# Optimization experiments

Hardware: AMD Instinct MI355X
Metric: run time of the kernel (lower is better)

## Reference

```python
import jax, jax.numpy as jnp
import numpy as np
from jax import lax

T = 32768
DUNITS = 1024
ATT_DIM = 512
EPROJS = 512
ACONV_CHANS = 32
ACONV_FILTS = 15  # kernel = 2*15+1 = 31


def setup_inputs() -> dict:
    key = jax.random.key(0)
    ks = jax.random.split(key, 8)
    dec_z = jax.random.normal(ks[0], (1, DUNITS), jnp.float32)
    att_prev = jax.random.uniform(ks[1], (1, T), jnp.float32)
    att_prev = att_prev / jnp.sum(att_prev, axis=1, keepdims=True)  # prob-like alignment
    pre_compute_enc_h = jax.random.normal(ks[2], (1, T, ATT_DIM), jnp.float32) * 0.1
    enc_h = jax.random.normal(ks[3], (1, T, EPROJS), jnp.float32)
    mask = jnp.zeros((1, T), jnp.float32)  # additive mask (0 = keep)
    conv_w = jax.random.normal(ks[4], (ACONV_CHANS, 1, 2 * ACONV_FILTS + 1), jnp.float32) * 0.1
    conv_b = jnp.zeros((ACONV_CHANS,), jnp.float32)
    W_att = jax.random.normal(ks[5], (ATT_DIM, ACONV_CHANS), jnp.float32) * 0.1
    W_dec = jax.random.normal(ks[6], (ATT_DIM, DUNITS), jnp.float32) * 0.03
    W_g = jax.random.normal(ks[7], (1, ATT_DIM), jnp.float32) * 0.05
    b_g = jnp.zeros((1,), jnp.float32)
    return {"dec_z": dec_z, "att_prev": att_prev, "pre_compute_enc_h": pre_compute_enc_h,
            "enc_h": enc_h, "mask": mask, "conv_w": conv_w, "conv_b": conv_b,
            "W_att": W_att, "W_dec": W_dec, "W_g": W_g, "b_g": b_g}


def reference(dec_z, att_prev, pre_compute_enc_h, enc_h, mask, conv_w, conv_b, W_att, W_dec, W_g, b_g):
    scaling = 2.0
    # location conv: att_prev [1,T] -> [1,C,T] (Conv2d with height-1 kernel == Conv1d)
    att_conv = lax.conv_general_dilated(
        att_prev[:, None, :], conv_w, window_strides=(1,),
        padding=[(ACONV_FILTS, ACONV_FILTS)],
        dimension_numbers=("NCH", "OIH", "NCH"))
    att_conv = att_conv + conv_b[None, :, None]          # [1,C,T]
    att_conv = jnp.einsum("bct,ac->bta", att_conv, W_att)  # mlp_att -> [1,T,att_dim]
    dec_z_tiled = (dec_z @ W_dec.T)[:, None, :]           # [1,1,att_dim]
    # gvec over tanh sum -> energies [1,T]
    e = jnp.einsum("bta,a->bt", jnp.tanh(pre_compute_enc_h + dec_z_tiled + att_conv), W_g[0]) + b_g[0]
    e = e + mask
    w = jax.nn.softmax(scaling * e, axis=1)               # [1,T]
    # forward-attention recurrence: shift-add-mul, then L1 normalize
    att_prev_shift = jnp.pad(att_prev, ((0, 0), (1, 0)))[:, :-1]
    w = (att_prev + att_prev_shift) * w
    w = jnp.clip(w, 1e-6, None)
    w = w / jnp.sum(w, axis=1, keepdims=True)             # L1 normalize (w > 0)
    c = jnp.sum(enc_h * w[:, :, None], axis=1)            # [1,eprojs]
    return (c, w)
```

## Files before the change

kernel.cpp:

```cpp
#include <hip/hip_runtime.h>

#define T_LEN 32768
#define ADIM  512
#define NDEC  1024
#define KTAPS 31

#define WS_BASE 0
#define WS_G    512
#define WS_SARR 16384
#define WS_BMAX 49152
#define WS_BSUM 51200
#define WS_SSUM 53248
#define WS_U    53504
#define WS_CREP 86272

typedef __attribute__((ext_vector_type(8))) short bf16x8;
typedef __attribute__((ext_vector_type(4))) float f32x4;

__device__ __forceinline__ float fast_tanh(float x) {
    float e = __expf(2.0f * x);
    return 1.0f - 2.0f * __builtin_amdgcn_rcpf(e + 1.0f);
}

__device__ __forceinline__ unsigned short f2bf(float f) {
    unsigned u = __float_as_uint(f);
    return (unsigned short)((u + 0x7FFFu + ((u >> 16) & 1u)) >> 16);
}

__global__ __launch_bounds__(256) void k0_prep(
        const float* __restrict__ dec_z, const float* __restrict__ conv_w,
        const float* __restrict__ conv_b, const float* __restrict__ W_att,
        const float* __restrict__ W_dec, float* __restrict__ ws) {
    int b = blockIdx.x, tid = threadIdx.x;
    int lane = tid & 63, wave = tid >> 6;
    if (b < 64) {
        if (b == 0 && tid == 0) ws[WS_SSUM] = 0.f;
        for (int s = 0; s < 2; ++s) {
            int a = b * 8 + wave * 2 + s;
            float sum = 0.f;
            #pragma unroll
            for (int i = 0; i < 16; ++i)
                sum += W_dec[a * NDEC + i * 64 + lane] * dec_z[i * 64 + lane];
            #pragma unroll
            for (int off = 32; off > 0; off >>= 1) sum += __shfl_xor(sum, off);
            if (lane == 0) {
                float bias = 0.f;
                #pragma unroll
                for (int c = 0; c < 32; ++c) bias += conv_b[c] * W_att[a * 32 + c];
                ws[WS_BASE + a] = sum + bias;
            }
        }
    } else {
        int k = b - 64;
        unsigned short* Gf = (unsigned short*)(ws + WS_G);
        for (int s = 0; s < 2; ++s) {
            int a = 2 * tid + s;
            float g = 0.f;
            if (k < KTAPS) {
                #pragma unroll
                for (int c = 0; c < 32; ++c)
                    g += conv_w[c * KTAPS + k] * W_att[a * 32 + c];
            }
            int at = a >> 4, col = a & 15;
            int l = col | ((k >> 3) << 4), i = k & 7;
            Gf[(at * 64 + l) * 8 + i] = f2bf(g);
        }
    }
}

__global__ __launch_bounds__(512, 8) void k1_energy(
        const float* __restrict__ att_prev, const float* __restrict__ pre,
        const float* __restrict__ mask, const float* __restrict__ W_g,
        const float* __restrict__ b_g, float* __restrict__ ws) {
    __shared__ float pre_s[16 * ADIM];
    __shared__ float ap_s[48];
    __shared__ float eP[8][16];
    int tid = threadIdx.x, lane = tid & 63, wave = tid >> 6;
    int t0 = blockIdx.x * 16;

    if (blockIdx.x < 32) ws[WS_CREP + blockIdx.x * 512 + tid] = 0.f;

    {
        const float* grow = pre + (size_t)(t0 + 2 * wave) * ADIM + lane * 4;
        float* lrow = &pre_s[(2 * wave) * ADIM];
        #pragma unroll
        for (int r = 0; r < 2; ++r) {
            #pragma unroll
            for (int h = 0; h < 2; ++h) {
                __builtin_amdgcn_global_load_lds(
                    (const __attribute__((address_space(1))) void*)(grow + r * ADIM + h * 256),
                    (__attribute__((address_space(3))) void*)(lrow + r * ADIM + h * 256),
                    16, 0, 0);
            }
        }
    }
    if (tid < 48) {
        int g = t0 - 15 + tid;
        ap_s[tid] = (g >= 0 && g < T_LEN) ? att_prev[g] : 0.f;
    }
    __syncthreads();

    int row = lane & 15, g4 = lane >> 4;

    bf16x8 afrag;
    int aidx = row + g4 * 8;
    #pragma unroll
    for (int i = 0; i < 8; ++i) afrag[i] = (short)f2bf(ap_s[aidx + i]);

    const unsigned short* Gf = (const unsigned short*)(ws + WS_G);
    float e_acc[4] = {0.f, 0.f, 0.f, 0.f};

    #pragma unroll 2
    for (int p = 0; p < 4; ++p) {
        int at = wave * 4 + p;
        int ac = at * 16 + row;
        bf16x8 bfrag = *(const bf16x8*)(Gf + (size_t)(at * 64 + lane) * 8);
        float bs = ws[WS_BASE + ac];
        f32x4 c = {bs, bs, bs, bs};
        c = __builtin_amdgcn_mfma_f32_16x16x32_bf16(afrag, bfrag, c, 0, 0, 0);
        float wgv = W_g[ac];
        #pragma unroll
        for (int r = 0; r < 4; ++r) {
            float pv = pre_s[(g4 * 4 + r) * ADIM + ac];
            e_acc[r] = fmaf(fast_tanh(c[r] + pv), wgv, e_acc[r]);
        }
    }

    #pragma unroll
    for (int r = 0; r < 4; ++r) {
        float s = e_acc[r];
        s += __shfl_xor(s, 1); s += __shfl_xor(s, 2);
        s += __shfl_xor(s, 4); s += __shfl_xor(s, 8);
        e_acc[r] = s;
    }
    if (row == 0) {
        #pragma unroll
        for (int r = 0; r < 4; ++r) eP[wave][g4 * 4 + r] = e_acc[r];
    }
    __syncthreads();

    if (wave == 0) {
        float sv = -1e30f, z0 = 0.f;
        if (lane < 16) {
            float e = 0.f;
            #pragma unroll
            for (int q = 0; q < 8; ++q) e += eP[q][lane];
            int t = t0 + lane;
            sv = 2.0f * (e + b_g[0] + mask[t]);
            ws[WS_SARR + t] = sv;
            z0 = 1.0f;
        }
        float m = sv, z = z0;
        #pragma unroll
        for (int off = 32; off > 0; off >>= 1) {
            float mo = __shfl_xor(m, off), zo = __shfl_xor(z, off);
            float mn = fmaxf(m, mo);
            z = z * __expf(m - mn) + zo * __expf(mo - mn);
            m = mn;
        }
        if (lane == 0) { ws[WS_BMAX + blockIdx.x] = m; ws[WS_BSUM + blockIdx.x] = z; }
    }
}

__global__ __launch_bounds__(512, 4) void k3_context(
        const float* __restrict__ att_prev, const float* __restrict__ enc_h,
        float* __restrict__ ws) {
    __shared__ float wmz[16];
    __shared__ float cbuf[4 * 512];
    int tid = threadIdx.x, lane = tid & 63, wave = tid >> 6;

    float mo[4], zo[4];
    #pragma unroll
    for (int k = 0; k < 4; ++k) {
        mo[k] = ws[WS_BMAX + (wave + 8 * k) * 64 + lane];
        zo[k] = ws[WS_BSUM + (wave + 8 * k) * 64 + lane];
    }
    float m = mo[0], z = zo[0];
    #pragma unroll
    for (int k = 1; k < 4; ++k) {
        float mn = fmaxf(m, mo[k]);
        z = z * __expf(m - mn) + zo[k] * __expf(mo[k] - mn);
        m = mn;
    }
    #pragma unroll
    for (int off = 32; off > 0; off >>= 1) {
        float mx = __shfl_xor(m, off), zx = __shfl_xor(z, off);
        float mn = fmaxf(m, mx);
        z = z * __expf(m - mn) + zx * __expf(mx - mn);
        m = mn;
    }
    if (lane == 0) { wmz[wave] = m; wmz[8 + wave] = z; }
    __syncthreads();
    float M = wmz[0], Z = wmz[8];
    #pragma unroll
    for (int w = 1; w < 8; ++w) {
        float mn = fmaxf(M, wmz[w]);
        Z = Z * __expf(M - mn) + wmz[8 + w] * __expf(wmz[w] - mn);
        M = mn;
    }
    float invZ = 1.0f / Z;

    int team = tid >> 7, l = tid & 127;
    int a4 = 4 * l;
    float4 acc = make_float4(0.f, 0.f, 0.f, 0.f);

    #pragma unroll 1
    for (int half = 0; half < 2; ++half) {
        int t0 = blockIdx.x * 64 + half * 32;
        int tb = t0 + team * 8;

        float u[8];
        #pragma unroll
        for (int i = 0; i < 8; ++i) {
            int t = tb + i;
            float ap0 = att_prev[t];
            float apm = (t > 0) ? att_prev[t - 1] : 0.f;
            u[i] = fmaxf((ap0 + apm) * __expf(ws[WS_SARR + t] - M) * invZ, 1e-6f);
        }
        float4 e[8];
        #pragma unroll
        for (int i = 0; i < 8; ++i)
            e[i] = *(const float4*)(enc_h + (size_t)(tb + i) * ADIM + a4);
        #pragma unroll
        for (int i = 0; i < 8; ++i) {
            acc.x = fmaf(u[i], e[i].x, acc.x);
            acc.y = fmaf(u[i], e[i].y, acc.y);
            acc.z = fmaf(u[i], e[i].z, acc.z);
            acc.w = fmaf(u[i], e[i].w, acc.w);
        }

        if (wave == 0 && lane < 32) {
            int t = t0 + lane;
            float ap0 = att_prev[t];
            float apm = (t > 0) ? att_prev[t - 1] : 0.f;
            float uu = fmaxf((ap0 + apm) * __expf(ws[WS_SARR + t] - M) * invZ, 1e-6f);
            ws[WS_U + t] = uu;
            float s = uu;
            #pragma unroll
            for (int off = 16; off > 0; off >>= 1) s += __shfl_xor(s, off, 32);
            if (lane == 0) atomicAdd(&ws[WS_SSUM], s);
        }
    }

    if (team != 0) *(float4*)&cbuf[team * 512 + a4] = acc;
    __syncthreads();
    if (team == 0) {
        float4 b1 = *(const float4*)&cbuf[1 * 512 + a4];
        float4 b2 = *(const float4*)&cbuf[2 * 512 + a4];
        float4 b3 = *(const float4*)&cbuf[3 * 512 + a4];
        float* rep = ws + WS_CREP + (blockIdx.x & 31) * 512;
        atomicAdd(&rep[a4 + 0], acc.x + b1.x + b2.x + b3.x);
        atomicAdd(&rep[a4 + 1], acc.y + b1.y + b2.y + b3.y);
        atomicAdd(&rep[a4 + 2], acc.z + b1.z + b2.z + b3.z);
        atomicAdd(&rep[a4 + 3], acc.w + b1.w + b2.w + b3.w);
    }
}

__global__ __launch_bounds__(512) void k4_final(
        const float* __restrict__ ws, float* __restrict__ out) {
    int b = blockIdx.x, tid = threadIdx.x;
    float invS = 1.0f / ws[WS_SSUM];
    if (b == 0) {
        float acc = 0.f;
        #pragma unroll
        for (int r = 0; r < 32; ++r) acc += ws[WS_CREP + r * 512 + tid];
        out[tid] = acc * invS;
    } else {
        int i = (b - 1) * 512 + tid;
        out[512 + i] = ws[WS_U + i] * invS;
    }
}

extern "C" void kernel_launch(void* const* d_in, const int* in_sizes, int n_in,
                              void* d_out, int out_size, void* d_ws, size_t ws_size,
                              hipStream_t stream) {
    const float* dec_z    = (const float*)d_in[0];
    const float* att_prev = (const float*)d_in[1];
    const float* pre      = (const float*)d_in[2];
    const float* enc_h    = (const float*)d_in[3];
    const float* mask     = (const float*)d_in[4];
    const float* conv_w   = (const float*)d_in[5];
    const float* conv_b   = (const float*)d_in[6];
    const float* W_att    = (const float*)d_in[7];
    const float* W_dec    = (const float*)d_in[8];
    const float* W_g      = (const float*)d_in[9];
    const float* b_g      = (const float*)d_in[10];
    float* out = (float*)d_out;
    float* ws  = (float*)d_ws;

    k0_prep   <<<96,   256, 0, stream>>>(dec_z, conv_w, conv_b, W_att, W_dec, ws);
    k1_energy <<<2048, 512, 0, stream>>>(att_prev, pre, mask, W_g, b_g, ws);
    k3_context<<<512,  512, 0, stream>>>(att_prev, enc_h, ws);
    k4_final  <<<65,   512, 0, stream>>>(ws, out);
}
```

Baseline: 181.8 us.

## Give each wave its own 16 timesteps with double-buffered LDS prefetch

Restructures the energy kernel so each wave owns 16 timesteps and walks all 512 attention columns in four chunks. Chunks of pre_compute_enc_h stream into per-wave double-buffered LDS through async global-to-LDS loads with explicit vmcnt waits. This overlaps memory traffic with MFMA and tanh work and removes block-level syncs and the cross-wave energy reduction. The cost is fewer, larger blocks (512 blocks of 256 threads), lower occupancy, and hand-placed waitcnt/sched_barrier ordering that must exactly match the outstanding loads.

```diff
diff --git a/kernel.cpp b/kernel.cpp
--- a/kernel.cpp
+++ b/kernel.cpp
@@ -26,6 +26,13 @@
     unsigned u = __float_as_uint(f);
     return (unsigned short)((u + 0x7FFFu + ((u >> 16) & 1u)) >> 16);
 }
+
+#define WAITV8()  do { asm volatile("s_waitcnt vmcnt(8)" ::: "memory"); \
+                       __builtin_amdgcn_sched_barrier(0); } while (0)
+#define WAITV0()  do { asm volatile("s_waitcnt vmcnt(0)" ::: "memory"); \
+                       __builtin_amdgcn_sched_barrier(0); } while (0)
+#define WAITL0()  do { asm volatile("s_waitcnt lgkmcnt(0)" ::: "memory"); \
+                       __builtin_amdgcn_sched_barrier(0); } while (0)
 
 __global__ __launch_bounds__(256) void k0_prep(
         const float* __restrict__ dec_z, const float* __restrict__ conv_w,
@@ -68,63 +75,84 @@
     }
 }
 
-__global__ __launch_bounds__(512, 8) void k1_energy(
+__global__ __launch_bounds__(256, 2) void k1_energy(
         const float* __restrict__ att_prev, const float* __restrict__ pre,
         const float* __restrict__ mask, const float* __restrict__ W_g,
         const float* __restrict__ b_g, float* __restrict__ ws) {
-    __shared__ float pre_s[16 * ADIM];
-    __shared__ float ap_s[48];
-    __shared__ float eP[8][16];
+    __shared__ float lds[4][2][2048];
     int tid = threadIdx.x, lane = tid & 63, wave = tid >> 6;
-    int t0 = blockIdx.x * 16;
-
-    if (blockIdx.x < 32) ws[WS_CREP + blockIdx.x * 512 + tid] = 0.f;
-
-    {
-        const float* grow = pre + (size_t)(t0 + 2 * wave) * ADIM + lane * 4;
-        float* lrow = &pre_s[(2 * wave) * ADIM];
-        #pragma unroll
-        for (int r = 0; r < 2; ++r) {
-            #pragma unroll
-            for (int h = 0; h < 2; ++h) {
-                __builtin_amdgcn_global_load_lds(
-                    (const __attribute__((address_space(1))) void*)(grow + r * ADIM + h * 256),
-                    (__attribute__((address_space(3))) void*)(lrow + r * ADIM + h * 256),
-                    16, 0, 0);
-            }
-        }
-    }
-    if (tid < 48) {
-        int g = t0 - 15 + tid;
-        ap_s[tid] = (g >= 0 && g < T_LEN) ? att_prev[g] : 0.f;
-    }
-    __syncthreads();
-
+    int W = blockIdx.x * 4 + wave;
+    int t0 = W * 16;
     int row = lane & 15, g4 = lane >> 4;
 
+    if (blockIdx.x < 64) ws[WS_CREP + blockIdx.x * 256 + tid] = 0.f;
+
+    const float* src0 = pre + (size_t)(t0 + (lane >> 5)) * ADIM + (lane & 31) * 4;
+
+#define STAGE(c, buf) do {                                                          \
+        const float* _s = src0 + (c) * 128;                                         \
+        _Pragma("unroll")                                                           \
+        for (int i = 0; i < 8; ++i) {                                               \
+            __builtin_amdgcn_global_load_lds(                                       \
+                (const __attribute__((address_space(1))) void*)(_s + (size_t)(2*i) * ADIM), \
+                (__attribute__((address_space(3))) void*)((buf) + i * 256),         \
+                16, 0, 0);                                                          \
+        }                                                                           \
+    } while (0)
+
     bf16x8 afrag;
-    int aidx = row + g4 * 8;
-    #pragma unroll
-    for (int i = 0; i < 8; ++i) afrag[i] = (short)f2bf(ap_s[aidx + i]);
-
+    int abase = t0 - 15 + row + g4 * 8;
+    #pragma unroll
+    for (int i = 0; i < 8; ++i) {
+        int idx = abase + i;
+        float v = (idx >= 0 && idx < T_LEN) ? att_prev[idx] : 0.f;
+        afrag[i] = (short)f2bf(v);
+    }
+
+    float* buf0 = &lds[wave][0][0];
+    float* buf1 = &lds[wave][1][0];
     const unsigned short* Gf = (const unsigned short*)(ws + WS_G);
     float e_acc[4] = {0.f, 0.f, 0.f, 0.f};
 
-    #pragma unroll 2
-    for (int p = 0; p < 4; ++p) {
-        int at = wave * 4 + p;
-        int ac = at * 16 + row;
-        bf16x8 bfrag = *(const bf16x8*)(Gf + (size_t)(at * 64 + lane) * 8);
-        float bs = ws[WS_BASE + ac];
-        f32x4 c = {bs, bs, bs, bs};
-        c = __builtin_amdgcn_mfma_f32_16x16x32_bf16(afrag, bfrag, c, 0, 0, 0);
-        float wgv = W_g[ac];
-        #pragma unroll
-        for (int r = 0; r < 4; ++r) {
-            float pv = pre_s[(g4 * 4 + r) * ADIM + ac];
-            e_acc[r] = fmaf(fast_tanh(c[r] + pv), wgv, e_acc[r]);
-        }
-    }
+#define COMPUTE(c, buf) do {                                                        \
+        _Pragma("unroll")                                                           \
+        for (int p = 0; p < 8; ++p) {                                               \
+            int at = (c) * 8 + p;                                                   \
+            int ac = at * 16 + row;                                                 \
+            bf16x8 bfrag = *(const bf16x8*)(Gf + (size_t)(at * 64 + lane) * 8);     \
+            float bs = ws[WS_BASE + ac];                                            \
+            f32x4 cc = {bs, bs, bs, bs};                                            \
+            cc = __builtin_amdgcn_mfma_f32_16x16x32_bf16(afrag, bfrag, cc, 0, 0, 0);\
+            float wgv = W_g[ac];                                                    \
+            _Pragma("unroll")                                                       \
+            for (int r = 0; r < 4; ++r) {                                           \
+                float pv = (buf)[(g4 * 4 + r) * 128 + p * 16 + row];                \
+                e_acc[r] = fmaf(fast_tanh(cc[r] + pv), wgv, e_acc[r]);              \
+            }                                                                       \
+        }                                                                           \
+    } while (0)
+
+    STAGE(0, buf0);
+    STAGE(1, buf1);
+
+    WAITV8();
+    COMPUTE(0, buf0);
+    WAITL0();
+    STAGE(2, buf0);
+
+    WAITV8();
+    COMPUTE(1, buf1);
+    WAITL0();
+    STAGE(3, buf1);
+
+    WAITV8();
+    COMPUTE(2, buf0);
+
+    WAITV0();
+    COMPUTE(3, buf1);
+
+#undef STAGE
+#undef COMPUTE
 
     #pragma unroll
     for (int r = 0; r < 4; ++r) {
@@ -133,33 +161,30 @@
         s += __shfl_xor(s, 4); s += __shfl_xor(s, 8);
         e_acc[r] = s;
     }
+
+    float bg = b_g[0];
+    float m = -1e30f, z = 0.f;
+    float sv[4];
+    #pragma unroll
+    for (int r = 0; r < 4; ++r) {
+        int t = t0 + g4 * 4 + r;
+        sv[r] = 2.0f * (e_acc[r] + bg + mask[t]);
+        float mn = fmaxf(m, sv[r]);
+        z = z * __expf(m - mn) + __expf(sv[r] - mn);
+        m = mn;
+    }
     if (row == 0) {
         #pragma unroll
-        for (int r = 0; r < 4; ++r) eP[wave][g4 * 4 + r] = e_acc[r];
-    }
-    __syncthreads();
-
-    if (wave == 0) {
-        float sv = -1e30f, z0 = 0.f;
-        if (lane < 16) {
-            float e = 0.f;
-            #pragma unroll
-            for (int q = 0; q < 8; ++q) e += eP[q][lane];
-            int t = t0 + lane;
-            sv = 2.0f * (e + b_g[0] + mask[t]);
-            ws[WS_SARR + t] = sv;
-            z0 = 1.0f;
-        }
-        float m = sv, z = z0;
-        #pragma unroll
-        for (int off = 32; off > 0; off >>= 1) {
-            float mo = __shfl_xor(m, off), zo = __shfl_xor(z, off);
-            float mn = fmaxf(m, mo);
-            z = z * __expf(m - mn) + zo * __expf(mo - mn);
-            m = mn;
-        }
-        if (lane == 0) { ws[WS_BMAX + blockIdx.x] = m; ws[WS_BSUM + blockIdx.x] = z; }
-    }
+        for (int r = 0; r < 4; ++r) ws[WS_SARR + t0 + g4 * 4 + r] = sv[r];
+    }
+    #pragma unroll
+    for (int off = 16; off <= 32; off <<= 1) {
+        float mo = __shfl_xor(m, off), zo = __shfl_xor(z, off);
+        float mn = fmaxf(m, mo);
+        z = z * __expf(m - mn) + zo * __expf(mo - mn);
+        m = mn;
+    }
+    if (lane == 0) { ws[WS_BMAX + W] = m; ws[WS_BSUM + W] = z; }
 }
 
 __global__ __launch_bounds__(512, 4) void k3_context(
@@ -288,8 +313,8 @@
     float* out = (float*)d_out;
     float* ws  = (float*)d_ws;
 
-    k0_prep   <<<96,   256, 0, stream>>>(dec_z, conv_w, conv_b, W_att, W_dec, ws);
-    k1_energy <<<2048, 512, 0, stream>>>(att_prev, pre, mask, W_g, b_g, ws);
-    k3_context<<<512,  512, 0, stream>>>(att_prev, enc_h, ws);
-    k4_final  <<<65,   512, 0, stream>>>(ws, out);
-}
+    k0_prep   <<<96,  256, 0, stream>>>(dec_z, conv_w, conv_b, W_att, W_dec, ws);
+    k1_energy <<<512, 256, 0, stream>>>(att_prev, pre, mask, W_g, b_g, ws);
+    k3_context<<<512, 512, 0, stream>>>(att_prev, enc_h, ws);
+    k4_final  <<<65,  512, 0, stream>>>(ws, out);
+}
```

Result: no change. 182.7 us (+0.5%).
